# Kernel optimization log

Hardware: AMD Instinct MI355X
Metric: run time of the kernel (lower is better)

Reference implementation:

```python
import jax, jax.numpy as jnp
import numpy as np

SEQ, BS, D, F, E = 1024, 2, 2048, 2048, 8


def setup_inputs() -> dict:
    key = jax.random.key(0)
    ks = jax.random.split(key, 8)
    s = 0.02  # param init scale
    return {
        "hidden_states": jax.random.normal(ks[0], (SEQ, BS, D), jnp.float32),
        "router_w": jax.random.normal(ks[1], (D, E), jnp.float32) * s,
        "gate_w": jax.random.normal(ks[2], (E, D, F), jnp.float32) * s,
        "up_w": jax.random.normal(ks[3], (E, D, F), jnp.float32) * s,
        "down_w": jax.random.normal(ks[4], (E, F, D), jnp.float32) * s,
        "shared_gate_w": jax.random.normal(ks[5], (D, F), jnp.float32) * s,
        "shared_up_w": jax.random.normal(ks[6], (D, F), jnp.float32) * s,
        "shared_down_w": jax.random.normal(ks[7], (F, D), jnp.float32) * s,
    }


def reference(hidden_states, router_w, gate_w, up_w, down_w,
              shared_gate_w, shared_up_w, shared_down_w):
    S, B, Dm = hidden_states.shape
    x = hidden_states.reshape(-1, Dm)          # [T, D] flattened tokens
    # --- router: top-1 expert, sigmoid gate applied to the selected logit ---
    logits = x @ router_w                      # [T, E]
    expert_idx = jnp.argmax(logits, axis=-1)   # top-1 index, [T]
    score = jax.nn.sigmoid(jnp.max(logits, axis=-1))  # [T]
    xs = x * score[:, None]                    # scale BEFORE expert (Llama4)
    # --- per-expert SwiGLU MLP on masked token sets, scatter-combined ---
    n_experts = router_w.shape[1]
    out = jnp.zeros_like(x)
    for e in range(n_experts):                 # small structural loop over experts
        m = (expert_idx == e)[:, None]
        xe = jnp.where(m, xs, 0.0)             # zeroed dispatch (equiv to gather)
        h = jax.nn.silu(xe @ gate_w[e]) * (xe @ up_w[e])
        out = out + jnp.where(m, h @ down_w[e], 0.0)
    # --- shared expert on all tokens ---
    shared = (jax.nn.silu(x @ shared_gate_w) * (x @ shared_up_w)) @ shared_down_w
    return (out + shared).reshape(S, B, Dm)
```

## Files before the change

### kernel.cpp

```cpp
#include <hip/hip_runtime.h>
#include <stdint.h>
#include <math.h>

#define T_TOK 2048
#define DIM   2048
#define FDIM  2048
#define NE    8

#define BM 64
#define BN 128
#define BK 32
#define MATSZ 4194304ull

typedef unsigned short u16;
typedef short s16x8 __attribute__((ext_vector_type(8)));
typedef float f32x4 __attribute__((ext_vector_type(4)));

__device__ __forceinline__ u16 f2bf(float f) {
    union { float f; unsigned int u; } v; v.f = f;
    unsigned int r = v.u + 0x7FFFu + ((v.u >> 16) & 1u);
    return (u16)(r >> 16);
}

__device__ __forceinline__ void gload_lds16(const void* g, void* l) {
    __builtin_amdgcn_global_load_lds((const __attribute__((address_space(1))) void*)g,
                                     (__attribute__((address_space(3))) void*)l, 16, 0, 0);
}

__global__ __launch_bounds__(256) void router_k(
    const float* __restrict__ x, const float* __restrict__ rw,
    float* __restrict__ score, int* __restrict__ eidx, int* __restrict__ counts)
{
    int t = blockIdx.x;
    int tid = threadIdx.x;
    float p[8] = {0.f,0.f,0.f,0.f,0.f,0.f,0.f,0.f};
    const float* xrow = x + (size_t)t * DIM;
    for (int d = tid; d < DIM; d += 256) {
        float xv = xrow[d];
        const float4* r = (const float4*)(rw + (size_t)d * 8);
        float4 r0 = r[0], r1 = r[1];
        p[0] += xv * r0.x; p[1] += xv * r0.y; p[2] += xv * r0.z; p[3] += xv * r0.w;
        p[4] += xv * r1.x; p[5] += xv * r1.y; p[6] += xv * r1.z; p[7] += xv * r1.w;
    }
    #pragma unroll
    for (int off = 32; off > 0; off >>= 1) {
        #pragma unroll
        for (int e = 0; e < 8; ++e) p[e] += __shfl_down(p[e], off);
    }
    __shared__ float red[4][8];
    int wave = tid >> 6, lane = tid & 63;
    if (lane == 0) {
        #pragma unroll
        for (int e = 0; e < 8; ++e) red[wave][e] = p[e];
    }
    __syncthreads();
    if (tid == 0) {
        float lg[8];
        #pragma unroll
        for (int e = 0; e < 8; ++e) lg[e] = red[0][e] + red[1][e] + red[2][e] + red[3][e];
        int best = 0; float bv = lg[0];
        #pragma unroll
        for (int e = 1; e < 8; ++e) { if (lg[e] > bv) { bv = lg[e]; best = e; } }
        score[t] = 1.f / (1.f + expf(-bv));
        eidx[t] = best;
        atomicAdd(&counts[best], 1);
    }
}

__global__ void scan_k(const int* __restrict__ counts, int* __restrict__ offs,
                       int* __restrict__ fill)
{
    if (threadIdx.x == 0 && blockIdx.x == 0) {
        int run = 0;
        for (int e = 0; e < NE; ++e) { offs[e] = run; fill[e] = run; run += counts[e]; }
    }
}

__global__ __launch_bounds__(256) void gather_k(
    const float* __restrict__ x, const float* __restrict__ score,
    const int* __restrict__ eidx, int* __restrict__ fill,
    int* __restrict__ tokmap, u16* __restrict__ xsc, u16* __restrict__ xbf)
{
    int t = blockIdx.x, tid = threadIdx.x;
    __shared__ int sp;
    if (tid == 0) {
        int e = eidx[t];
        int p = atomicAdd(&fill[e], 1);
        tokmap[p] = t;
        sp = p;
    }
    __syncthreads();
    int pos = sp;
    float s = score[t];
    const float4* xr = (const float4*)(x + (size_t)t * DIM);
    float4 a = xr[tid * 2], b = xr[tid * 2 + 1];
    alignas(16) u16 raw[8] = { f2bf(a.x), f2bf(a.y), f2bf(a.z), f2bf(a.w),
                               f2bf(b.x), f2bf(b.y), f2bf(b.z), f2bf(b.w) };
    alignas(16) u16 scl[8] = { f2bf(a.x*s), f2bf(a.y*s), f2bf(a.z*s), f2bf(a.w*s),
                               f2bf(b.x*s), f2bf(b.y*s), f2bf(b.z*s), f2bf(b.w*s) };
    *(s16x8*)(xbf + (size_t)t * DIM + tid * 8)   = *(s16x8*)raw;
    *(s16x8*)(xsc + (size_t)pos * DIM + tid * 8) = *(s16x8*)scl;
}

#define TLDS 260
__global__ __launch_bounds__(256) void wtrans_k(
    const float* __restrict__ gw, const float* __restrict__ uw,
    const float* __restrict__ dwn, const float* __restrict__ sgw,
    const float* __restrict__ suw, const float* __restrict__ sdw,
    u16* __restrict__ wt, int mstart)
{
    int bid = blockIdx.x;
    int m = mstart + (bid >> 8);
    int kt = (bid >> 3) & 31;
    int nt = bid & 7;
    const float* src;
    if      (m < 8)   src = gw  + (size_t)m * MATSZ;
    else if (m < 16)  src = uw  + (size_t)(m - 8) * MATSZ;
    else if (m == 16) src = sgw;
    else if (m == 17) src = suw;
    else if (m < 26)  src = dwn + (size_t)(m - 18) * MATSZ;
    else              src = sdw;
    u16* dst = wt + (size_t)m * MATSZ;

    int k0 = kt * 64, n0 = nt * 256;
    __shared__ u16 T[64 * TLDS];
    int t = threadIdx.x;
    int lw = t >> 6, l = t & 63;

    #pragma unroll 4
    for (int i = 0; i < 16; ++i) {
        int kk = lw * 16 + i;
        float4 v = *(const float4*)&src[(size_t)(k0 + kk) * 2048 + n0 + l * 4];
        alignas(8) u16 b4[4] = { f2bf(v.x), f2bf(v.y), f2bf(v.z), f2bf(v.w) };
        *(uint64_t*)&T[kk * TLDS + l * 4] = *(uint64_t*)b4;
    }
    __syncthreads();

    int c  = t & 7;
    int nb = t >> 3;
    #pragma unroll
    for (int p = 0; p < 8; ++p) {
        int n = p * 32 + nb;
        alignas(16) u16 o[8];
        #pragma unroll
        for (int jj = 0; jj < 8; ++jj) {
            int j = (jj + c) & 7;
            o[j] = T[(c * 8 + j) * TLDS + n];
        }
        *(s16x8*)&dst[(size_t)(n0 + n) * 2048 + k0 + c * 8] = *(s16x8*)o;
    }
}

__global__ __launch_bounds__(256) void gateup_k(
    const u16* __restrict__ xsc, const u16* __restrict__ xbf,
    const u16* __restrict__ wt,
    const int* __restrict__ counts, const int* __restrict__ offs,
    u16* __restrict__ Hbf, u16* __restrict__ Hs)
{
    int bid = blockIdx.x;
    int g  = bid >> 9;
    int mt = (bid >> 4) & 31;
    int nt = bid & 15;

    int M; const u16* A; const u16* Wg; const u16* Wu; u16* Ho;
    if (g < NE) {
        M = counts[g];
        int ro = offs[g];
        A  = xsc + (size_t)ro * DIM;
        Wg = wt + (size_t)g * MATSZ;
        Wu = wt + (size_t)(8 + g) * MATSZ;
        Ho = Hbf + (size_t)ro * FDIM;
    } else {
        M = T_TOK; A = xbf;
        Wg = wt + 16 * MATSZ;
        Wu = wt + 17 * MATSZ;
        Ho = Hs;
    }
    int m0 = mt * BM;
    if (m0 >= M) return;
    int n0 = nt * BN;

    __shared__ __align__(128) u16 As[BM * BK];
    __shared__ __align__(128) u16 Bg[BN * BK];
    __shared__ __align__(128) u16 Bu[BN * BK];

    int tid = threadIdx.x;
    int l   = tid & 63;
    int w   = tid >> 6;
    int wm = (w >> 1) * 32;
    int wn = (w & 1) * 64;

    f32x4 accg[2][4], accu[2][4];
    #pragma unroll
    for (int i = 0; i < 2; ++i)
        #pragma unroll
        for (int j = 0; j < 4; ++j) { accg[i][j] = (f32x4)0.f; accu[i][j] = (f32x4)0.f; }

    int rr = l >> 2;
    int co = (l & 3) * 8;
    const u16* gA   = A  + (size_t)min(m0 + w * 16 + rr, M - 1) * DIM + co;
    const u16* gBg0 = Wg + (size_t)(n0 + w * 16 + rr)      * DIM + co;
    const u16* gBg1 = Wg + (size_t)(n0 + 64 + w * 16 + rr) * DIM + co;
    const u16* gBu0 = Wu + (size_t)(n0 + w * 16 + rr)      * DIM + co;
    const u16* gBu1 = Wu + (size_t)(n0 + 64 + w * 16 + rr) * DIM + co;
    u16* lA   = As + (w * 16) * BK;
    u16* lBg0 = Bg + (w * 16) * BK;
    u16* lBg1 = Bg + (64 + w * 16) * BK;
    u16* lBu0 = Bu + (w * 16) * BK;
    u16* lBu1 = Bu + (64 + w * 16) * BK;

    int am   = wm + (l & 15);
    int koff = (l >> 4) * 8;

    for (int k0 = 0; k0 < DIM; k0 += BK) {
        gload_lds16(gA,   lA);
        gload_lds16(gBg0, lBg0); gload_lds16(gBg1, lBg1);
        gload_lds16(gBu0, lBu0); gload_lds16(gBu1, lBu1);
        gA += BK; gBg0 += BK; gBg1 += BK; gBu0 += BK; gBu1 += BK;
        __syncthreads();

        s16x8 af0 = *(const s16x8*)&As[am * BK + koff];
        s16x8 af1 = *(const s16x8*)&As[(am + 16) * BK + koff];
        #pragma unroll
        for (int j = 0; j < 4; ++j) {
            int bc = wn + j * 16 + (l & 15);
            s16x8 bg = *(const s16x8*)&Bg[bc * BK + koff];
            s16x8 bu = *(const s16x8*)&Bu[bc * BK + koff];
            accg[0][j] = __builtin_amdgcn_mfma_f32_16x16x32_bf16(af0, bg, accg[0][j], 0, 0, 0);
            accg[1][j] = __builtin_amdgcn_mfma_f32_16x16x32_bf16(af1, bg, accg[1][j], 0, 0, 0);
            accu[0][j] = __builtin_amdgcn_mfma_f32_16x16x32_bf16(af0, bu, accu[0][j], 0, 0, 0);
            accu[1][j] = __builtin_amdgcn_mfma_f32_16x16x32_bf16(af1, bu, accu[1][j], 0, 0, 0);
        }
        __syncthreads();
    }

    int rbase = wm + ((l >> 4) << 2);
    int cbase = n0 + wn + (l & 15);
    #pragma unroll
    for (int i = 0; i < 2; ++i) {
        #pragma unroll
        for (int j = 0; j < 4; ++j) {
            #pragma unroll
            for (int r = 0; r < 4; ++r) {
                int row = m0 + rbase + i * 16 + r;
                if (row < M) {
                    float gv = accg[i][j][r];
                    float uv = accu[i][j][r];
                    float h = gv / (1.f + expf(-gv)) * uv;
                    Ho[(size_t)row * FDIM + cbase + j * 16] = f2bf(h);
                }
            }
        }
    }
}

__global__ __launch_bounds__(256) void down_k(
    const u16* __restrict__ Hbf, const u16* __restrict__ Hs,
    const u16* __restrict__ wt,
    const int* __restrict__ counts, const int* __restrict__ offs,
    const int* __restrict__ tokmap, float* __restrict__ out, int shared_pass)
{
    int bid = blockIdx.x;
    int g, mt, nt, M, ro; const u16* A; const u16* W;
    if (shared_pass) {
        g = NE; mt = bid >> 4; nt = bid & 15;
        M = T_TOK; ro = 0; A = Hs; W = wt + 26 * MATSZ;
    } else {
        g = bid >> 9; mt = (bid >> 4) & 31; nt = bid & 15;
        M = counts[g]; ro = offs[g];
        A = Hbf + (size_t)ro * FDIM;
        W = wt + (size_t)(18 + g) * MATSZ;
    }
    int m0 = mt * BM;
    if (m0 >= M) return;
    int n0 = nt * BN;

    __shared__ __align__(128) u16 As[BM * BK];
    __shared__ __align__(128) u16 Bd[BN * BK];

    int tid = threadIdx.x;
    int l   = tid & 63;
    int w   = tid >> 6;
    int wm = (w >> 1) * 32;
    int wn = (w & 1) * 64;

    f32x4 acc[2][4];
    #pragma unroll
    for (int i = 0; i < 2; ++i)
        #pragma unroll
        for (int j = 0; j < 4; ++j) acc[i][j] = (f32x4)0.f;

    int rr = l >> 2;
    int co = (l & 3) * 8;
    const u16* gA  = A + (size_t)min(m0 + w * 16 + rr, M - 1) * FDIM + co;
    const u16* gB0 = W + (size_t)(n0 + w * 16 + rr)      * FDIM + co;
    const u16* gB1 = W + (size_t)(n0 + 64 + w * 16 + rr) * FDIM + co;
    u16* lA  = As + (w * 16) * BK;
    u16* lB0 = Bd + (w * 16) * BK;
    u16* lB1 = Bd + (64 + w * 16) * BK;

    int am   = wm + (l & 15);
    int koff = (l >> 4) * 8;

    for (int k0 = 0; k0 < FDIM; k0 += BK) {
        gload_lds16(gA, lA);
        gload_lds16(gB0, lB0); gload_lds16(gB1, lB1);
        gA += BK; gB0 += BK; gB1 += BK;
        __syncthreads();

        s16x8 af0 = *(const s16x8*)&As[am * BK + koff];
        s16x8 af1 = *(const s16x8*)&As[(am + 16) * BK + koff];
        #pragma unroll
        for (int j = 0; j < 4; ++j) {
            int bc = wn + j * 16 + (l & 15);
            s16x8 bd = *(const s16x8*)&Bd[bc * BK + koff];
            acc[0][j] = __builtin_amdgcn_mfma_f32_16x16x32_bf16(af0, bd, acc[0][j], 0, 0, 0);
            acc[1][j] = __builtin_amdgcn_mfma_f32_16x16x32_bf16(af1, bd, acc[1][j], 0, 0, 0);
        }
        __syncthreads();
    }

    int rbase = wm + ((l >> 4) << 2);
    int cbase = n0 + wn + (l & 15);
    #pragma unroll
    for (int i = 0; i < 2; ++i) {
        #pragma unroll
        for (int r = 0; r < 4; ++r) {
            int row = m0 + rbase + i * 16 + r;
            if (row < M) {
                if (shared_pass) {
                    float* dst = out + (size_t)row * DIM;
                    #pragma unroll
                    for (int j = 0; j < 4; ++j) dst[cbase + j * 16] = acc[i][j][r];
                } else {
                    float* dst = out + (size_t)tokmap[ro + row] * DIM;
                    #pragma unroll
                    for (int j = 0; j < 4; ++j)
                        dst[cbase + j * 16] = dst[cbase + j * 16] + acc[i][j][r];
                }
            }
        }
    }
}

extern "C" void kernel_launch(void* const* d_in, const int* in_sizes, int n_in,
                              void* d_out, int out_size, void* d_ws, size_t ws_size,
                              hipStream_t stream) {
    const float* x   = (const float*)d_in[0];
    const float* rw  = (const float*)d_in[1];
    const float* gw  = (const float*)d_in[2];
    const float* uw  = (const float*)d_in[3];
    const float* dwn = (const float*)d_in[4];
    const float* sgw = (const float*)d_in[5];
    const float* suw = (const float*)d_in[6];
    const float* sdw = (const float*)d_in[7];
    float* out = (float*)d_out;

    char* ws = (char*)d_ws;
    float* score = (float*)(ws);
    int* eidx    = (int*)(ws + 8192);
    int* counts  = (int*)(ws + 16384);
    int* fill    = (int*)(ws + 16448);
    int* offs    = (int*)(ws + 16512);
    int* tokmap  = (int*)(ws + 16576);
    u16* xsc = (u16*)(ws + 32768);
    u16* xbf = xsc + MATSZ;
    u16* Hbf = xbf + MATSZ;
    u16* Hs  = Hbf + MATSZ;
    u16* wt  = (u16*)(ws + 32768 + 4ull * 8388608 + 16777216);

    hipMemsetAsync(counts, 0, 128, stream);

    router_k<<<T_TOK, 256, 0, stream>>>(x, rw, score, eidx, counts);
    scan_k<<<1, 64, 0, stream>>>(counts, offs, fill);
    gather_k<<<T_TOK, 256, 0, stream>>>(x, score, eidx, fill, tokmap, xsc, xbf);

    wtrans_k<<<18 * 256, 256, 0, stream>>>(gw, uw, dwn, sgw, suw, sdw, wt, 0);
    gateup_k<<<9 * 512, 256, 0, stream>>>(xsc, xbf, wt, counts, offs, Hbf, Hs);

    wtrans_k<<<9 * 256, 256, 0, stream>>>(gw, uw, dwn, sgw, suw, sdw, wt, 18);
    down_k<<<512, 256, 0, stream>>>(Hbf, Hs, wt, counts, offs, tokmap, out, 1);
    down_k<<<8 * 512, 256, 0, stream>>>(Hbf, Hs, wt, counts, offs, tokmap, out, 0);
}
```

Measured before the change: 731.6 us.

## Fuse fp32 weight conversion into GEMM loads and enlarge M tile

Removes the separate weight transpose/convert kernels and has the gate/up and down GEMMs read fp32 weights directly. They convert to bf16 in registers and write into a padded, XOR-swizzled LDS layout. The M tile doubles to 128 rows, so each block reuses B fragments across four A fragments and the grids shrink. This avoids a full extra read/write pass over all 27 weight matrices. In exchange, the GEMM loads fp32 weights (twice the bytes) through registers instead of async LDS loads, and each weight tile is converted once per M-tile.

Result: slower. 838.6 us (+14.6%).

```diff
diff --git a/kernel.cpp b/kernel.cpp
--- a/kernel.cpp
+++ b/kernel.cpp
@@ -1,4 +1,5 @@
 #include <hip/hip_runtime.h>
+#include <hip/hip_bf16.h>
 #include <stdint.h>
 #include <math.h>
 
@@ -7,19 +8,29 @@
 #define FDIM  2048
 #define NE    8
 
-#define BM 64
+#define BM 128
 #define BN 128
 #define BK 32
+#define BROW 36
 #define MATSZ 4194304ull
 
 typedef unsigned short u16;
+typedef unsigned int u32;
 typedef short s16x8 __attribute__((ext_vector_type(8)));
+typedef short s16x4 __attribute__((ext_vector_type(4)));
 typedef float f32x4 __attribute__((ext_vector_type(4)));
+typedef unsigned int u32x2 __attribute__((ext_vector_type(2)));
 
 __device__ __forceinline__ u16 f2bf(float f) {
     union { float f; unsigned int u; } v; v.f = f;
     unsigned int r = v.u + 0x7FFFu + ((v.u >> 16) & 1u);
     return (u16)(r >> 16);
+}
+
+__device__ __forceinline__ u32 pkbf(float a, float b) {
+    union { __hip_bfloat162 h; u32 u; } v;
+    v.h = __float22bfloat162_rn(make_float2(a, b));
+    return v.u;
 }
 
 __device__ __forceinline__ void gload_lds16(const void* g, void* l) {
@@ -102,241 +113,242 @@
     *(s16x8*)(xsc + (size_t)pos * DIM + tid * 8) = *(s16x8*)scl;
 }
 
-#define TLDS 260
-__global__ __launch_bounds__(256) void wtrans_k(
+__global__ __launch_bounds__(256) void gateup2_k(
+    const u16* __restrict__ xsc, const u16* __restrict__ xbf,
     const float* __restrict__ gw, const float* __restrict__ uw,
-    const float* __restrict__ dwn, const float* __restrict__ sgw,
-    const float* __restrict__ suw, const float* __restrict__ sdw,
-    u16* __restrict__ wt, int mstart)
-{
-    int bid = blockIdx.x;
-    int m = mstart + (bid >> 8);
-    int kt = (bid >> 3) & 31;
-    int nt = bid & 7;
-    const float* src;
-    if      (m < 8)   src = gw  + (size_t)m * MATSZ;
-    else if (m < 16)  src = uw  + (size_t)(m - 8) * MATSZ;
-    else if (m == 16) src = sgw;
-    else if (m == 17) src = suw;
-    else if (m < 26)  src = dwn + (size_t)(m - 18) * MATSZ;
-    else              src = sdw;
-    u16* dst = wt + (size_t)m * MATSZ;
-
-    int k0 = kt * 64, n0 = nt * 256;
-    __shared__ u16 T[64 * TLDS];
-    int t = threadIdx.x;
-    int lw = t >> 6, l = t & 63;
-
-    #pragma unroll 4
-    for (int i = 0; i < 16; ++i) {
-        int kk = lw * 16 + i;
-        float4 v = *(const float4*)&src[(size_t)(k0 + kk) * 2048 + n0 + l * 4];
-        alignas(8) u16 b4[4] = { f2bf(v.x), f2bf(v.y), f2bf(v.z), f2bf(v.w) };
-        *(uint64_t*)&T[kk * TLDS + l * 4] = *(uint64_t*)b4;
-    }
-    __syncthreads();
-
-    int c  = t & 7;
-    int nb = t >> 3;
-    #pragma unroll
-    for (int p = 0; p < 8; ++p) {
-        int n = p * 32 + nb;
-        alignas(16) u16 o[8];
-        #pragma unroll
-        for (int jj = 0; jj < 8; ++jj) {
-            int j = (jj + c) & 7;
-            o[j] = T[(c * 8 + j) * TLDS + n];
-        }
-        *(s16x8*)&dst[(size_t)(n0 + n) * 2048 + k0 + c * 8] = *(s16x8*)o;
-    }
-}
-
-__global__ __launch_bounds__(256) void gateup_k(
-    const u16* __restrict__ xsc, const u16* __restrict__ xbf,
-    const u16* __restrict__ wt,
+    const float* __restrict__ sgw, const float* __restrict__ suw,
     const int* __restrict__ counts, const int* __restrict__ offs,
     u16* __restrict__ Hbf, u16* __restrict__ Hs)
 {
     int bid = blockIdx.x;
-    int g  = bid >> 9;
-    int mt = (bid >> 4) & 31;
+    int g  = bid >> 8;
+    int mt = (bid >> 4) & 15;
     int nt = bid & 15;
 
-    int M; const u16* A; const u16* Wg; const u16* Wu; u16* Ho;
+    int M; const u16* A; const float* Wg; const float* Wu; u16* Ho;
     if (g < NE) {
         M = counts[g];
         int ro = offs[g];
         A  = xsc + (size_t)ro * DIM;
-        Wg = wt + (size_t)g * MATSZ;
-        Wu = wt + (size_t)(8 + g) * MATSZ;
+        Wg = gw + (size_t)g * MATSZ;
+        Wu = uw + (size_t)g * MATSZ;
         Ho = Hbf + (size_t)ro * FDIM;
     } else {
-        M = T_TOK; A = xbf;
-        Wg = wt + 16 * MATSZ;
-        Wu = wt + 17 * MATSZ;
-        Ho = Hs;
+        M = T_TOK; A = xbf; Wg = sgw; Wu = suw; Ho = Hs;
     }
     int m0 = mt * BM;
     if (m0 >= M) return;
     int n0 = nt * BN;
 
     __shared__ __align__(128) u16 As[BM * BK];
-    __shared__ __align__(128) u16 Bg[BN * BK];
-    __shared__ __align__(128) u16 Bu[BN * BK];
+    __shared__ __align__(128) u16 Bgs[BN * BROW];
+    __shared__ __align__(128) u16 Bus[BN * BROW];
 
     int tid = threadIdx.x;
-    int l   = tid & 63;
-    int w   = tid >> 6;
-    int wm = (w >> 1) * 32;
+    int l = tid & 63;
+    int w = tid >> 6;
+    int wm = (w >> 1) * 64;
     int wn = (w & 1) * 64;
 
-    f32x4 accg[2][4], accu[2][4];
-    #pragma unroll
-    for (int i = 0; i < 2; ++i)
+    f32x4 accg[4][4], accu[4][4];
+    #pragma unroll
+    for (int i = 0; i < 4; ++i)
         #pragma unroll
         for (int j = 0; j < 4; ++j) { accg[i][j] = (f32x4)0.f; accu[i][j] = (f32x4)0.f; }
 
-    int rr = l >> 2;
-    int co = (l & 3) * 8;
-    const u16* gA   = A  + (size_t)min(m0 + w * 16 + rr, M - 1) * DIM + co;
-    const u16* gBg0 = Wg + (size_t)(n0 + w * 16 + rr)      * DIM + co;
-    const u16* gBg1 = Wg + (size_t)(n0 + 64 + w * 16 + rr) * DIM + co;
-    const u16* gBu0 = Wu + (size_t)(n0 + w * 16 + rr)      * DIM + co;
-    const u16* gBu1 = Wu + (size_t)(n0 + 64 + w * 16 + rr) * DIM + co;
-    u16* lA   = As + (w * 16) * BK;
-    u16* lBg0 = Bg + (w * 16) * BK;
-    u16* lBg1 = Bg + (64 + w * 16) * BK;
-    u16* lBu0 = Bu + (w * 16) * BK;
-    u16* lBu1 = Bu + (64 + w * 16) * BK;
+    const u16* gA0 = A + (size_t)min(m0 + w*32 +      (l>>2), M-1)*DIM + (l&3)*8;
+    const u16* gA1 = A + (size_t)min(m0 + w*32 + 16 + (l>>2), M-1)*DIM + (l&3)*8;
+    u16* lA0 = As + (w*32)      * BK;
+    u16* lA1 = As + (w*32 + 16) * BK;
+
+    int n4 = tid & 31;
+    int kq = tid >> 5;
+    int slot = (kq ^ ((n4 >> 2) & 7)) << 2;
+    const float* gBg = Wg + (size_t)(kq*4)*FDIM + n0 + n4*4;
+    const float* gBu = Wu + (size_t)(kq*4)*FDIM + n0 + n4*4;
+    u16* wBg = Bgs + (n4*4)*BROW + slot;
+    u16* wBu = Bus + (n4*4)*BROW + slot;
 
     int am   = wm + (l & 15);
     int koff = (l >> 4) * 8;
+    int q0   = (l >> 4) * 2;
+    int wnq  = wn >> 4;
 
     for (int k0 = 0; k0 < DIM; k0 += BK) {
-        gload_lds16(gA,   lA);
-        gload_lds16(gBg0, lBg0); gload_lds16(gBg1, lBg1);
-        gload_lds16(gBu0, lBu0); gload_lds16(gBu1, lBu1);
-        gA += BK; gBg0 += BK; gBg1 += BK; gBu0 += BK; gBu1 += BK;
         __syncthreads();
-
-        s16x8 af0 = *(const s16x8*)&As[am * BK + koff];
+        gload_lds16(gA0, lA0);
+        gload_lds16(gA1, lA1);
+        gA0 += BK; gA1 += BK;
+        f32x4 b0 = *(const f32x4*)(gBg);
+        f32x4 b1 = *(const f32x4*)(gBg + FDIM);
+        f32x4 b2 = *(const f32x4*)(gBg + 2*FDIM);
+        f32x4 b3 = *(const f32x4*)(gBg + 3*FDIM);
+        f32x4 c0 = *(const f32x4*)(gBu);
+        f32x4 c1 = *(const f32x4*)(gBu + FDIM);
+        f32x4 c2 = *(const f32x4*)(gBu + 2*FDIM);
+        f32x4 c3 = *(const f32x4*)(gBu + 3*FDIM);
+        gBg += (size_t)BK * FDIM; gBu += (size_t)BK * FDIM;
+        #pragma unroll
+        for (int j = 0; j < 4; ++j) {
+            u32x2 vg = { pkbf(b0[j], b1[j]), pkbf(b2[j], b3[j]) };
+            u32x2 vu = { pkbf(c0[j], c1[j]), pkbf(c2[j], c3[j]) };
+            *(u32x2*)(wBg + j*BROW) = vg;
+            *(u32x2*)(wBu + j*BROW) = vu;
+        }
+        __syncthreads();
+
+        s16x8 af0 = *(const s16x8*)&As[(am     ) * BK + koff];
         s16x8 af1 = *(const s16x8*)&As[(am + 16) * BK + koff];
-        #pragma unroll
-        for (int j = 0; j < 4; ++j) {
-            int bc = wn + j * 16 + (l & 15);
-            s16x8 bg = *(const s16x8*)&Bg[bc * BK + koff];
-            s16x8 bu = *(const s16x8*)&Bu[bc * BK + koff];
-            accg[0][j] = __builtin_amdgcn_mfma_f32_16x16x32_bf16(af0, bg, accg[0][j], 0, 0, 0);
-            accg[1][j] = __builtin_amdgcn_mfma_f32_16x16x32_bf16(af1, bg, accg[1][j], 0, 0, 0);
-            accu[0][j] = __builtin_amdgcn_mfma_f32_16x16x32_bf16(af0, bu, accu[0][j], 0, 0, 0);
-            accu[1][j] = __builtin_amdgcn_mfma_f32_16x16x32_bf16(af1, bu, accu[1][j], 0, 0, 0);
-        }
-        __syncthreads();
-    }
-
-    int rbase = wm + ((l >> 4) << 2);
+        s16x8 af2 = *(const s16x8*)&As[(am + 32) * BK + koff];
+        s16x8 af3 = *(const s16x8*)&As[(am + 48) * BK + koff];
+        #pragma unroll
+        for (int j = 0; j < 4; ++j) {
+            int bc = wn + j*16 + (l & 15);
+            int sj = (wnq + j) & 7;
+            const u16* rg = &Bgs[bc * BROW];
+            const u16* ru = &Bus[bc * BROW];
+            s16x4 glo = *(const s16x4*)(rg + (((q0    ) ^ sj) << 2));
+            s16x4 ghi = *(const s16x4*)(rg + (((q0 + 1) ^ sj) << 2));
+            s16x4 ulo = *(const s16x4*)(ru + (((q0    ) ^ sj) << 2));
+            s16x4 uhi = *(const s16x4*)(ru + (((q0 + 1) ^ sj) << 2));
+            s16x8 bgf = __builtin_shufflevector(glo, ghi, 0,1,2,3,4,5,6,7);
+            s16x8 buf_ = __builtin_shufflevector(ulo, uhi, 0,1,2,3,4,5,6,7);
+            accg[0][j] = __builtin_amdgcn_mfma_f32_16x16x32_bf16(af0, bgf, accg[0][j], 0, 0, 0);
+            accg[1][j] = __builtin_amdgcn_mfma_f32_16x16x32_bf16(af1, bgf, accg[1][j], 0, 0, 0);
+            accg[2][j] = __builtin_amdgcn_mfma_f32_16x16x32_bf16(af2, bgf, accg[2][j], 0, 0, 0);
+            accg[3][j] = __builtin_amdgcn_mfma_f32_16x16x32_bf16(af3, bgf, accg[3][j], 0, 0, 0);
+            accu[0][j] = __builtin_amdgcn_mfma_f32_16x16x32_bf16(af0, buf_, accu[0][j], 0, 0, 0);
+            accu[1][j] = __builtin_amdgcn_mfma_f32_16x16x32_bf16(af1, buf_, accu[1][j], 0, 0, 0);
+            accu[2][j] = __builtin_amdgcn_mfma_f32_16x16x32_bf16(af2, buf_, accu[2][j], 0, 0, 0);
+            accu[3][j] = __builtin_amdgcn_mfma_f32_16x16x32_bf16(af3, buf_, accu[3][j], 0, 0, 0);
+        }
+    }
+
+    int rbase = m0 + wm + ((l >> 4) << 2);
     int cbase = n0 + wn + (l & 15);
     #pragma unroll
-    for (int i = 0; i < 2; ++i) {
+    for (int i = 0; i < 4; ++i) {
         #pragma unroll
         for (int j = 0; j < 4; ++j) {
             #pragma unroll
             for (int r = 0; r < 4; ++r) {
-                int row = m0 + rbase + i * 16 + r;
+                int row = rbase + i*16 + r;
                 if (row < M) {
                     float gv = accg[i][j][r];
                     float uv = accu[i][j][r];
                     float h = gv / (1.f + expf(-gv)) * uv;
-                    Ho[(size_t)row * FDIM + cbase + j * 16] = f2bf(h);
+                    Ho[(size_t)row * FDIM + cbase + j*16] = f2bf(h);
                 }
             }
         }
     }
 }
 
-__global__ __launch_bounds__(256) void down_k(
+__global__ __launch_bounds__(256) void down2_k(
     const u16* __restrict__ Hbf, const u16* __restrict__ Hs,
-    const u16* __restrict__ wt,
+    const float* __restrict__ dwn, const float* __restrict__ sdw,
     const int* __restrict__ counts, const int* __restrict__ offs,
     const int* __restrict__ tokmap, float* __restrict__ out, int shared_pass)
 {
     int bid = blockIdx.x;
-    int g, mt, nt, M, ro; const u16* A; const u16* W;
+    int mt, nt, M, ro; const u16* A; const float* W;
     if (shared_pass) {
-        g = NE; mt = bid >> 4; nt = bid & 15;
-        M = T_TOK; ro = 0; A = Hs; W = wt + 26 * MATSZ;
+        mt = bid >> 4; nt = bid & 15;
+        M = T_TOK; ro = 0; A = Hs; W = sdw;
     } else {
-        g = bid >> 9; mt = (bid >> 4) & 31; nt = bid & 15;
+        int g = bid >> 8; mt = (bid >> 4) & 15; nt = bid & 15;
         M = counts[g]; ro = offs[g];
         A = Hbf + (size_t)ro * FDIM;
-        W = wt + (size_t)(18 + g) * MATSZ;
+        W = dwn + (size_t)g * MATSZ;
     }
     int m0 = mt * BM;
     if (m0 >= M) return;
     int n0 = nt * BN;
 
     __shared__ __align__(128) u16 As[BM * BK];
-    __shared__ __align__(128) u16 Bd[BN * BK];
+    __shared__ __align__(128) u16 Bds[BN * BROW];
 
     int tid = threadIdx.x;
-    int l   = tid & 63;
-    int w   = tid >> 6;
-    int wm = (w >> 1) * 32;
+    int l = tid & 63;
+    int w = tid >> 6;
+    int wm = (w >> 1) * 64;
     int wn = (w & 1) * 64;
 
-    f32x4 acc[2][4];
-    #pragma unroll
-    for (int i = 0; i < 2; ++i)
+    f32x4 acc[4][4];
+    #pragma unroll
+    for (int i = 0; i < 4; ++i)
         #pragma unroll
         for (int j = 0; j < 4; ++j) acc[i][j] = (f32x4)0.f;
 
-    int rr = l >> 2;
-    int co = (l & 3) * 8;
-    const u16* gA  = A + (size_t)min(m0 + w * 16 + rr, M - 1) * FDIM + co;
-    const u16* gB0 = W + (size_t)(n0 + w * 16 + rr)      * FDIM + co;
-    const u16* gB1 = W + (size_t)(n0 + 64 + w * 16 + rr) * FDIM + co;
-    u16* lA  = As + (w * 16) * BK;
-    u16* lB0 = Bd + (w * 16) * BK;
-    u16* lB1 = Bd + (64 + w * 16) * BK;
+    const u16* gA0 = A + (size_t)min(m0 + w*32 +      (l>>2), M-1)*FDIM + (l&3)*8;
+    const u16* gA1 = A + (size_t)min(m0 + w*32 + 16 + (l>>2), M-1)*FDIM + (l&3)*8;
+    u16* lA0 = As + (w*32)      * BK;
+    u16* lA1 = As + (w*32 + 16) * BK;
+
+    int n4 = tid & 31;
+    int kq = tid >> 5;
+    int slot = (kq ^ ((n4 >> 2) & 7)) << 2;
+    const float* gB = W + (size_t)(kq*4)*DIM + n0 + n4*4;
+    u16* wB = Bds + (n4*4)*BROW + slot;
 
     int am   = wm + (l & 15);
     int koff = (l >> 4) * 8;
+    int q0   = (l >> 4) * 2;
+    int wnq  = wn >> 4;
 
     for (int k0 = 0; k0 < FDIM; k0 += BK) {
-        gload_lds16(gA, lA);
-        gload_lds16(gB0, lB0); gload_lds16(gB1, lB1);
-        gA += BK; gB0 += BK; gB1 += BK;
         __syncthreads();
-
-        s16x8 af0 = *(const s16x8*)&As[am * BK + koff];
+        gload_lds16(gA0, lA0);
+        gload_lds16(gA1, lA1);
+        gA0 += BK; gA1 += BK;
+        f32x4 b0 = *(const f32x4*)(gB);
+        f32x4 b1 = *(const f32x4*)(gB + DIM);
+        f32x4 b2 = *(const f32x4*)(gB + 2*DIM);
+        f32x4 b3 = *(const f32x4*)(gB + 3*DIM);
+        gB += (size_t)BK * DIM;
+        #pragma unroll
+        for (int j = 0; j < 4; ++j) {
+            u32x2 vb = { pkbf(b0[j], b1[j]), pkbf(b2[j], b3[j]) };
+            *(u32x2*)(wB + j*BROW) = vb;
+        }
+        __syncthreads();
+
+        s16x8 af0 = *(const s16x8*)&As[(am     ) * BK + koff];
         s16x8 af1 = *(const s16x8*)&As[(am + 16) * BK + koff];
-        #pragma unroll
-        for (int j = 0; j < 4; ++j) {
-            int bc = wn + j * 16 + (l & 15);
-            s16x8 bd = *(const s16x8*)&Bd[bc * BK + koff];
-            acc[0][j] = __builtin_amdgcn_mfma_f32_16x16x32_bf16(af0, bd, acc[0][j], 0, 0, 0);
-            acc[1][j] = __builtin_amdgcn_mfma_f32_16x16x32_bf16(af1, bd, acc[1][j], 0, 0, 0);
-        }
-        __syncthreads();
-    }
-
-    int rbase = wm + ((l >> 4) << 2);
+        s16x8 af2 = *(const s16x8*)&As[(am + 32) * BK + koff];
+        s16x8 af3 = *(const s16x8*)&As[(am + 48) * BK + koff];
+        #pragma unroll
+        for (int j = 0; j < 4; ++j) {
+            int bc = wn + j*16 + (l & 15);
+            int sj = (wnq + j) & 7;
+            const u16* rb = &Bds[bc * BROW];
+            s16x4 blo = *(const s16x4*)(rb + (((q0    ) ^ sj) << 2));
+            s16x4 bhi = *(const s16x4*)(rb + (((q0 + 1) ^ sj) << 2));
+            s16x8 bdf = __builtin_shufflevector(blo, bhi, 0,1,2,3,4,5,6,7);
+            acc[0][j] = __builtin_amdgcn_mfma_f32_16x16x32_bf16(af0, bdf, acc[0][j], 0, 0, 0);
+            acc[1][j] = __builtin_amdgcn_mfma_f32_16x16x32_bf16(af1, bdf, acc[1][j], 0, 0, 0);
+            acc[2][j] = __builtin_amdgcn_mfma_f32_16x16x32_bf16(af2, bdf, acc[2][j], 0, 0, 0);
+            acc[3][j] = __builtin_amdgcn_mfma_f32_16x16x32_bf16(af3, bdf, acc[3][j], 0, 0, 0);
+        }
+    }
+
+    int rbase = m0 + wm + ((l >> 4) << 2);
     int cbase = n0 + wn + (l & 15);
     #pragma unroll
-    for (int i = 0; i < 2; ++i) {
+    for (int i = 0; i < 4; ++i) {
         #pragma unroll
         for (int r = 0; r < 4; ++r) {
-            int row = m0 + rbase + i * 16 + r;
+            int row = rbase + i*16 + r;
             if (row < M) {
                 if (shared_pass) {
                     float* dst = out + (size_t)row * DIM;
                     #pragma unroll
-                    for (int j = 0; j < 4; ++j) dst[cbase + j * 16] = acc[i][j][r];
+                    for (int j = 0; j < 4; ++j) dst[cbase + j*16] = acc[i][j][r];
                 } else {
                     float* dst = out + (size_t)tokmap[ro + row] * DIM;
                     #pragma unroll
                     for (int j = 0; j < 4; ++j)
-                        dst[cbase + j * 16] = dst[cbase + j * 16] + acc[i][j][r];
+                        dst[cbase + j*16] = dst[cbase + j*16] + acc[i][j][r];
                 }
             }
         }
@@ -367,7 +379,6 @@
     u16* xbf = xsc + MATSZ;
     u16* Hbf = xbf + MATSZ;
     u16* Hs  = Hbf + MATSZ;
-    u16* wt  = (u16*)(ws + 32768 + 4ull * 8388608 + 16777216);
 
     hipMemsetAsync(counts, 0, 128, stream);
 
@@ -375,10 +386,7 @@
     scan_k<<<1, 64, 0, stream>>>(counts, offs, fill);
     gather_k<<<T_TOK, 256, 0, stream>>>(x, score, eidx, fill, tokmap, xsc, xbf);
 
-    wtrans_k<<<18 * 256, 256, 0, stream>>>(gw, uw, dwn, sgw, suw, sdw, wt, 0);
-    gateup_k<<<9 * 512, 256, 0, stream>>>(xsc, xbf, wt, counts, offs, Hbf, Hs);
-
-    wtrans_k<<<9 * 256, 256, 0, stream>>>(gw, uw, dwn, sgw, suw, sdw, wt, 18);
-    down_k<<<512, 256, 0, stream>>>(Hbf, Hs, wt, counts, offs, tokmap, out, 1);
-    down_k<<<8 * 512, 256, 0, stream>>>(Hbf, Hs, wt, counts, offs, tokmap, out, 0);
-}
+    gateup2_k<<<9 * 256, 256, 0, stream>>>(xsc, xbf, gw, uw, sgw, suw, counts, offs, Hbf, Hs);
+    down2_k<<<256, 256, 0, stream>>>(Hbf, Hs, dwn, sdw, counts, offs, tokmap, out, 1);
+    down2_k<<<8 * 256, 256, 0, stream>>>(Hbf, Hs, dwn, sdw, counts, offs, tokmap, out, 0);
+}
```
